# Performance work log

Hardware: AMD Instinct MI355X
Metric: run time of the kernel (lower is better)

The kernel has to match this reference:

```python
import jax, jax.numpy as jnp
import numpy as np

EMBED_DIM = 1024
NUM_HEADS = 8
SEQ_LEN = 2048
EPS = 1e-6


def setup_inputs() -> dict:
    key = jax.random.key(0)
    ks = jax.random.split(key, 8)
    E, NH, S = EMBED_DIM, NUM_HEADS, SEQ_LEN
    q = jax.random.normal(ks[0], (S, E), jnp.float32)
    k = jax.random.normal(ks[1], (S, E), jnp.float32)
    v = jax.random.normal(ks[2], (S, E), jnp.float32)
    # gate projections: weights init'd to zeros in the module; use small random
    # values so the gate math is exercised. Biases follow the module's init.
    Wi = 0.02 * jax.random.normal(ks[3], (NH, 3 * E), jnp.float32)
    bi = jnp.linspace(3.0, 6.0, NH, dtype=jnp.float32)
    Wf = 0.02 * jax.random.normal(ks[4], (NH, 3 * E), jnp.float32)
    bf = jnp.sqrt(0.1) * jax.random.normal(ks[5], (NH,), jnp.float32)
    # ResidualLayerNorm (xLSTM-style): effective scale = 1 + weight, no bias
    ln_weight = jnp.zeros((E,), jnp.float32)
    return {"q": q, "k": k, "v": v, "Wi": Wi, "bi": bi, "Wf": Wf, "bf": bf,
            "ln_weight": ln_weight}


def _mlstm_parallel(q, k, v, Wi, bi, Wf, bf, ln_weight):
    S, E = q.shape
    NH = Wi.shape[0]
    DH = E // NH
    gate_in = jnp.concatenate((q, k, v), axis=1)            # (S, 3E)
    ig = (gate_in @ Wi.T + bi).T[:, :, None]                # (NH, S, 1)
    fg = (gate_in @ Wf.T + bf).T[:, :, None]                # (NH, S, 1)

    qh = q.reshape(S, NH, DH).transpose(1, 0, 2)            # (NH, S, DH)
    kh = k.reshape(S, NH, DH).transpose(1, 0, 2)
    vh = v.reshape(S, NH, DH).transpose(1, 0, 2)

    # cumulative log forget gates
    log_f = jax.nn.log_sigmoid(fg)                          # (NH, S, 1)
    log_f_cum = jnp.concatenate(
        [jnp.zeros((NH, 1, 1), q.dtype), jnp.cumsum(log_f, axis=1)], axis=1
    )                                                       # (NH, S+1, 1)
    log_fg_mat = log_f_cum - log_f_cum.transpose(0, 2, 1)   # (NH, S+1, S+1)
    causal = jnp.tril(jnp.ones((S, S), bool))
    log_fg_mat = jnp.where(causal, log_fg_mat[:, 1:, 1:], -jnp.inf)  # (NH,S,S)

    log_D = log_fg_mat + ig.transpose(0, 2, 1)              # (NH, S, S)
    max_log_D = jnp.max(log_D, axis=-1, keepdims=True)      # (NH, S, 1)
    D = jnp.exp(log_D - max_log_D)                          # stabilized

    qk = jnp.einsum('hsd,htd->hst', qh, kh) / jnp.sqrt(jnp.asarray(DH, q.dtype))
    C = qk * D                                              # (NH, S, S)
    normalizer = jnp.maximum(jnp.abs(jnp.sum(C, axis=-1, keepdims=True)),
                             jnp.exp(-max_log_D))
    C_norm = C / (normalizer + EPS)
    h = jnp.einsum('hst,htd->hsd', C_norm, vh)              # (NH, S, DH)
    h = h.transpose(1, 0, 2).reshape(S, E)

    # residual layer norm: LN(h) * (1 + weight), no bias
    mu = jnp.mean(h, axis=-1, keepdims=True)
    var = jnp.mean(jnp.square(h - mu), axis=-1, keepdims=True)
    h_norm = (h - mu) * jax.lax.rsqrt(var + 1e-5)
    return h_norm * (1.0 + ln_weight)


def reference(q, k, v, Wi, bi, Wf, bf, ln_weight):
    return _mlstm_parallel(q, k, v, Wi, bi, Wf, bf, ln_weight)
```

## Files before the change

### kernel.cpp

```cpp
#include <hip/hip_runtime.h>
#include <math.h>

#define S_LEN 2048
#define EMB   1024
#define NHEAD 8
#define DH    128
#define E3    3072
#define BM    64
#define BN    32
#define NSPLIT 4
#define KSTRIDE  136
#define VTSTRIDE 40
#define PTSTRIDE 40

typedef __bf16 bf16x8 __attribute__((ext_vector_type(8)));
typedef __bf16 bf16x4 __attribute__((ext_vector_type(4)));
typedef float  f32x4  __attribute__((ext_vector_type(4)));

__global__ __launch_bounds__(256) void gates_cvt_transpose_kernel(
    const float* __restrict__ q, const float* __restrict__ k,
    const float* __restrict__ v,
    const float* __restrict__ Wi, const float* __restrict__ bi,
    const float* __restrict__ Wf, const float* __restrict__ bf,
    __bf16* __restrict__ Qh, __bf16* __restrict__ Ql,
    __bf16* __restrict__ Kh, __bf16* __restrict__ Kl,
    __bf16* __restrict__ Vt,
    float* __restrict__ ig, float* __restrict__ lf)
{
    const int tid = threadIdx.x;
    __shared__ union {
        float red[16][4];
        __bf16 tile[32][33];
    } sh;

    if (blockIdx.x < S_LEN) {
        const int t = blockIdx.x;
        const float4 qv = ((const float4*)q)[(size_t)t * 256 + tid];
        const float4 kv = ((const float4*)k)[(size_t)t * 256 + tid];
        const float4 vv = ((const float4*)v)[(size_t)t * 256 + tid];
        {
            size_t idx = (size_t)t * 256 + tid;
            bf16x4 hi, lo;
            hi[0]=(__bf16)qv.x; hi[1]=(__bf16)qv.y; hi[2]=(__bf16)qv.z; hi[3]=(__bf16)qv.w;
            lo[0]=(__bf16)(qv.x-(float)hi[0]); lo[1]=(__bf16)(qv.y-(float)hi[1]);
            lo[2]=(__bf16)(qv.z-(float)hi[2]); lo[3]=(__bf16)(qv.w-(float)hi[3]);
            ((bf16x4*)Qh)[idx] = hi; ((bf16x4*)Ql)[idx] = lo;
            hi[0]=(__bf16)kv.x; hi[1]=(__bf16)kv.y; hi[2]=(__bf16)kv.z; hi[3]=(__bf16)kv.w;
            lo[0]=(__bf16)(kv.x-(float)hi[0]); lo[1]=(__bf16)(kv.y-(float)hi[1]);
            lo[2]=(__bf16)(kv.z-(float)hi[2]); lo[3]=(__bf16)(kv.w-(float)hi[3]);
            ((bf16x4*)Kh)[idx] = hi; ((bf16x4*)Kl)[idx] = lo;
        }
        float acc[16];
        #pragma unroll
        for (int g = 0; g < 16; ++g) {
            const float4* w4 = (const float4*)((g < 8) ? (Wi + g * E3) : (Wf + (g - 8) * E3));
            float4 a = w4[tid], b = w4[256 + tid], c = w4[512 + tid];
            acc[g] = a.x*qv.x + a.y*qv.y + a.z*qv.z + a.w*qv.w
                   + b.x*kv.x + b.y*kv.y + b.z*kv.z + b.w*kv.w
                   + c.x*vv.x + c.y*vv.y + c.z*vv.z + c.w*vv.w;
        }
        const int w = tid >> 6, lane = tid & 63;
        #pragma unroll
        for (int g = 0; g < 16; ++g) {
            float x = acc[g];
            for (int o = 32; o > 0; o >>= 1) x += __shfl_down(x, o, 64);
            if (lane == 0) sh.red[g][w] = x;
        }
        __syncthreads();
        if (tid < 16) {
            float s = sh.red[tid][0] + sh.red[tid][1] + sh.red[tid][2] + sh.red[tid][3];
            if (tid < 8) {
                ig[tid * S_LEN + t] = s + bi[tid];
            } else {
                int h = tid - 8;
                float x = s + bf[h];
                lf[h * S_LEN + t] = fminf(x, 0.f) - log1pf(expf(-fabsf(x)));
            }
        }
    } else {
        const int tb = blockIdx.x - S_LEN;
        const int sb = (tb & 63) * 32, eb = (tb >> 6) * 32;
        #pragma unroll
        for (int i = 0; i < 4; ++i) {
            int lin = tid + i * 256;
            int sr = lin >> 5, ec = lin & 31;
            sh.tile[ec][sr] = (__bf16)v[(size_t)(sb + sr) * EMB + eb + ec];
        }
        __syncthreads();
        #pragma unroll
        for (int i = 0; i < 4; ++i) {
            int lin = tid + i * 256;
            int er = lin >> 5, sc = lin & 31;
            Vt[(size_t)(eb + er) * S_LEN + sb + sc] = sh.tile[er][sc];
        }
    }
}

__global__ __launch_bounds__(256) void cumsum_aux_kernel(
    const float* __restrict__ lf, const float* __restrict__ ig,
    float* __restrict__ F, float* __restrict__ ug,
    float* __restrict__ umax, float* __restrict__ upmax)
{
    const int h = blockIdx.x, tid = threadIdx.x;
    const int lane = tid & 63, w = tid >> 6;
    __shared__ float wsum[4];
    __shared__ float morig[256];
    float loc[8];
    const int base = tid * 8;
    float s = 0.f;
    for (int i = 0; i < 8; i++) { s += lf[h * S_LEN + base + i]; loc[i] = s; }
    float inc = s;
    #pragma unroll
    for (int o = 1; o < 64; o <<= 1) {
        float t = __shfl_up(inc, o, 64);
        if (lane >= o) inc += t;
    }
    if (lane == 63) wsum[w] = inc;
    __syncthreads();
    float wpre = 0.f;
    #pragma unroll
    for (int i = 0; i < 4; ++i) if (i < w) wpre += wsum[i];
    const float prev = wpre + inc - s;
    float* Fh = F + h * (S_LEN + 1);
    if (tid == 0) Fh[0] = 0.f;
    float Fv[8];
    for (int i = 0; i < 8; i++) { Fv[i] = prev + loc[i]; Fh[base + i + 1] = Fv[i]; }

    const float* igh = ig + h * S_LEN;
    float pm[8];
    float runm = -1e30f;
    #pragma unroll
    for (int i = 0; i < 8; i++) {
        float u = igh[base + i] - Fv[i];
        ug[h * S_LEN + base + i] = u;
        runm = fmaxf(runm, u);
        pm[i] = runm;
    }
    morig[tid] = runm;
    __syncthreads();
    const int g0 = tid & ~3;
    float pfx = -1e30f;
    for (int j = g0; j < tid; ++j) pfx = fmaxf(pfx, morig[j]);
    #pragma unroll
    for (int i = 0; i < 8; i++)
        upmax[h * S_LEN + base + i] = fmaxf(pfx, pm[i]);
    if ((tid & 3) == 0) {
        float mm = fmaxf(fmaxf(morig[tid], morig[tid + 1]),
                         fmaxf(morig[tid + 2], morig[tid + 3]));
        umax[h * 64 + (tid >> 2)] = mm;
    }
}

__global__ __launch_bounds__(256, 2) void mlstm_mfma(
    const __bf16* __restrict__ Qhg, const __bf16* __restrict__ Qlg,
    const __bf16* __restrict__ Khg, const __bf16* __restrict__ Klg,
    const __bf16* __restrict__ Vtg,
    const float* __restrict__ ug, const float* __restrict__ umaxg,
    const float* __restrict__ upmaxg, const float* __restrict__ F,
    __bf16* __restrict__ Opart, float* __restrict__ msplit,
    float* __restrict__ lsplit)
{
    const int flat = blockIdx.x;
    const int h = flat & 7;
    const int rest = flat >> 3;
    const int xx = rest & 15, z = rest >> 4;
    const int tid  = threadIdx.x;
    const int lane = tid & 63, w = tid >> 6;
    const int quad = lane >> 4, l15 = lane & 15;

    __shared__ __bf16 Kh[BN * KSTRIDE], Kl[BN * KSTRIDE];
    __shared__ __bf16 Vt[DH * VTSTRIDE];
    __shared__ __bf16 Pt[4][16 * PTSTRIDE];

    const float* Fh  = F  + h * (S_LEN + 1);
    const float* ugh = ug + h * S_LEN;
    const float scale = 0.088388347648318447f;
    const int kr  = tid >> 4, kc8 = tid & 15;
    const int vr0 = tid >> 2, vc0 = tid & 3;

    for (int pair = 0; pair < 2; ++pair) {
        const int qt = (pair == 0) ? xx : 31 - xx;
        const int qb = qt * BM;
        const int nj = 2 * qt + 2;
        const int j0 = (z * nj) / NSPLIT, j1 = ((z + 1) * nj) / NSPLIT;
        const int qbw = qb + w * 16;
        const int SBLK = (qb >> 5) + (w >> 1);

        float fq[4], upm[4];
        int sglob[4];
        #pragma unroll
        for (int r = 0; r < 4; ++r) {
            int s = qbw + quad * 4 + r;
            sglob[r] = s;
            fq[r]  = Fh[s + 1];
            upm[r] = upmaxg[h * S_LEN + s];
        }

        bf16x8 qh[4], ql[4];
        {
            const size_t qrow = (size_t)(qbw + l15) * EMB + h * DH + quad * 8;
            #pragma unroll
            for (int kk = 0; kk < 4; ++kk) {
                qh[kk] = *(const bf16x8*)(Qhg + qrow + kk * 32);
                ql[kk] = *(const bf16x8*)(Qlg + qrow + kk * 32);
            }
        }
        #pragma unroll
        for (int kk = 0; kk < 4; ++kk)
            asm volatile("" : "+v"(qh[kk]), "+v"(ql[kk]));

        float m_r[4] = {-1e30f, -1e30f, -1e30f, -1e30f};
        float l_r[4] = {0.f, 0.f, 0.f, 0.f};
        f32x4 Oacc[8] = {{0,0,0,0},{0,0,0,0},{0,0,0,0},{0,0,0,0},
                         {0,0,0,0},{0,0,0,0},{0,0,0,0},{0,0,0,0}};

        bf16x8 pk[2], pl[2], pv[2];
        float pu0 = 0.f, pu1 = 0.f, pum = 0.f;
        if (j0 < j1) {
            const int tb = j0 * BN;
            #pragma unroll
            for (int i = 0; i < 2; ++i) {
                int row = kr + 16 * i;
                size_t g = (size_t)(tb + row) * EMB + h * DH + kc8 * 8;
                pk[i] = *(const bf16x8*)(Khg + g);
                pl[i] = *(const bf16x8*)(Klg + g);
                pv[i] = *(const bf16x8*)(Vtg + (size_t)(h * DH + vr0 + 64 * i) * S_LEN + tb + vc0 * 8);
            }
            pu0 = ugh[tb + l15];
            pu1 = ugh[tb + 16 + l15];
            pum = umaxg[h * 64 + j0];
        }

        for (int j = j0; j < j1; ++j) {
            const int tb = j * BN;
            __syncthreads();
            #pragma unroll
            for (int i = 0; i < 2; ++i) {
                int row = kr + 16 * i;
                *(bf16x8*)&Kh[row * KSTRIDE + kc8 * 8] = pk[i];
                *(bf16x8*)&Kl[row * KSTRIDE + kc8 * 8] = pl[i];
                *(bf16x8*)&Vt[(vr0 + 64 * i) * VTSTRIDE + vc0 * 8] = pv[i];
            }
            __syncthreads();
            const float ut0 = pu0, ut1 = pu1, umj = pum;
            if (j + 1 < j1) {
                const int tb2 = tb + BN;
                #pragma unroll
                for (int i = 0; i < 2; ++i) {
                    int row = kr + 16 * i;
                    size_t g = (size_t)(tb2 + row) * EMB + h * DH + kc8 * 8;
                    pk[i] = *(const bf16x8*)(Khg + g);
                    pl[i] = *(const bf16x8*)(Klg + g);
                    pv[i] = *(const bf16x8*)(Vtg + (size_t)(h * DH + vr0 + 64 * i) * S_LEN + tb2 + vc0 * 8);
                }
                pu0 = ugh[tb2 + l15];
                pu1 = ugh[tb2 + 16 + l15];
                pum = umaxg[h * 64 + (j + 1)];
            }
            if (j <= SBLK) {
                f32x4 S0 = {0,0,0,0}, S1 = {0,0,0,0};
                #pragma unroll
                for (int kk = 0; kk < 4; ++kk) {
                    const int co = kk * 32 + quad * 8;
                    bf16x8 bh0 = *(const bf16x8*)&Kh[l15 * KSTRIDE + co];
                    bf16x8 bl0 = *(const bf16x8*)&Kl[l15 * KSTRIDE + co];
                    S0 = __builtin_amdgcn_mfma_f32_16x16x32_bf16(qh[kk], bh0, S0, 0, 0, 0);
                    S0 = __builtin_amdgcn_mfma_f32_16x16x32_bf16(qh[kk], bl0, S0, 0, 0, 0);
                    S0 = __builtin_amdgcn_mfma_f32_16x16x32_bf16(ql[kk], bh0, S0, 0, 0, 0);
                    bf16x8 bh1 = *(const bf16x8*)&Kh[(16 + l15) * KSTRIDE + co];
                    bf16x8 bl1 = *(const bf16x8*)&Kl[(16 + l15) * KSTRIDE + co];
                    S1 = __builtin_amdgcn_mfma_f32_16x16x32_bf16(qh[kk], bh1, S1, 0, 0, 0);
                    S1 = __builtin_amdgcn_mfma_f32_16x16x32_bf16(qh[kk], bl1, S1, 0, 0, 0);
                    S1 = __builtin_amdgcn_mfma_f32_16x16x32_bf16(ql[kk], bh1, S1, 0, 0, 0);
                }
                const int t0 = tb + l15, t1 = tb + 16 + l15;
                #pragma unroll
                for (int r = 0; r < 4; ++r) {
                    float mt = (j < SBLK) ? (fq[r] + umj) : (fq[r] + upm[r]);
                    float mn = fmaxf(m_r[r], mt);
                    float alpha = __expf(m_r[r] - mn);
                    m_r[r] = mn;
                    #pragma unroll
                    for (int nt = 0; nt < 8; ++nt) Oacc[nt][r] *= alpha;
                    float p0 = __expf(fq[r] + ut0 - mn) * S0[r] * scale;
                    float p1 = __expf(fq[r] + ut1 - mn) * S1[r] * scale;
                    if (j == SBLK) {
                        if (t0 > sglob[r]) p0 = 0.f;
                        if (t1 > sglob[r]) p1 = 0.f;
                    }
                    l_r[r] = l_r[r] * alpha + (p0 + p1);
                    const int prow = (quad * 4 + r) * PTSTRIDE;
                    Pt[w][prow + l15]      = (__bf16)p0;
                    Pt[w][prow + 16 + l15] = (__bf16)p1;
                }
                bf16x8 pa = *(const bf16x8*)&Pt[w][l15 * PTSTRIDE + quad * 8];
                #pragma unroll
                for (int nt = 0; nt < 8; ++nt) {
                    bf16x8 vb = *(const bf16x8*)&Vt[(nt * 16 + l15) * VTSTRIDE + quad * 8];
                    Oacc[nt] = __builtin_amdgcn_mfma_f32_16x16x32_bf16(pa, vb, Oacc[nt], 0, 0, 0);
                }
            }
        }
        __bf16* Oz = Opart + (size_t)z * S_LEN * EMB;
        #pragma unroll
        for (int nt = 0; nt < 8; ++nt) {
            #pragma unroll
            for (int r = 0; r < 4; ++r) {
                Oz[(size_t)sglob[r] * EMB + h * DH + nt * 16 + l15] = (__bf16)Oacc[nt][r];
            }
        }
        #pragma unroll
        for (int r = 0; r < 4; ++r) {
            float x = l_r[r];
            #pragma unroll
            for (int o = 1; o < 16; o <<= 1) x += __shfl_xor(x, o);
            l_r[r] = x;
        }
        if (l15 == 0) {
            #pragma unroll
            for (int r = 0; r < 4; ++r) {
                msplit[(z * NHEAD + h) * S_LEN + sglob[r]] = m_r[r];
                lsplit[(z * NHEAD + h) * S_LEN + sglob[r]] = l_r[r];
            }
        }
    }
}

__global__ __launch_bounds__(256) void combine_ln_kernel(
    const __bf16* __restrict__ Opart, const float* __restrict__ msplit,
    const float* __restrict__ lsplit, const float* __restrict__ lnw,
    float* __restrict__ out)
{
    const int tid = threadIdx.x;
    const int r  = tid >> 7;
    const int wr = (tid >> 6) & 1;
    const int c0 = (tid & 127) * 8;
    const int hh = c0 >> 7;
    const int s  = blockIdx.x * 2 + r;
    __shared__ float redsum[2][2], redvar[2][2];

    float m = -1e30f, es[NSPLIT], l = 0.f;
    #pragma unroll
    for (int zz = 0; zz < NSPLIT; ++zz)
        m = fmaxf(m, msplit[(zz * NHEAD + hh) * S_LEN + s]);
    #pragma unroll
    for (int zz = 0; zz < NSPLIT; ++zz) {
        es[zz] = __expf(msplit[(zz * NHEAD + hh) * S_LEN + s] - m);
        l += es[zz] * lsplit[(zz * NHEAD + hh) * S_LEN + s];
    }
    const float rn = 1.f / (fmaxf(fabsf(l), __expf(-m)) + 1e-6f);

    const size_t SE = (size_t)S_LEN * EMB;
    float x[8] = {0,0,0,0,0,0,0,0};
    #pragma unroll
    for (int zz = 0; zz < NSPLIT; ++zz) {
        bf16x8 o = *(const bf16x8*)(Opart + zz * SE + (size_t)s * EMB + c0);
        #pragma unroll
        for (int e = 0; e < 8; ++e) x[e] += es[zz] * (float)o[e];
    }
    float sum = 0.f;
    #pragma unroll
    for (int e = 0; e < 8; ++e) { x[e] *= rn; sum += x[e]; }
    for (int o = 32; o > 0; o >>= 1) sum += __shfl_down(sum, o, 64);
    if ((tid & 63) == 0) redsum[r][wr] = sum;
    __syncthreads();
    sum = redsum[r][0] + redsum[r][1];
    const float mu = sum * (1.f / EMB);
    float vs = 0.f;
    #pragma unroll
    for (int e = 0; e < 8; ++e) { float d = x[e] - mu; vs += d * d; }
    for (int o = 32; o > 0; o >>= 1) vs += __shfl_down(vs, o, 64);
    if ((tid & 63) == 0) redvar[r][wr] = vs;
    __syncthreads();
    vs = redvar[r][0] + redvar[r][1];
    const float rstd = rsqrtf(vs * (1.f / EMB) + 1e-5f);
    const float4 w0 = *(const float4*)(lnw + c0);
    const float4 w1 = *(const float4*)(lnw + c0 + 4);
    float4 o0, o1;
    o0.x = (x[0]-mu)*rstd*(1.f+w0.x); o0.y = (x[1]-mu)*rstd*(1.f+w0.y);
    o0.z = (x[2]-mu)*rstd*(1.f+w0.z); o0.w = (x[3]-mu)*rstd*(1.f+w0.w);
    o1.x = (x[4]-mu)*rstd*(1.f+w1.x); o1.y = (x[5]-mu)*rstd*(1.f+w1.y);
    o1.z = (x[6]-mu)*rstd*(1.f+w1.z); o1.w = (x[7]-mu)*rstd*(1.f+w1.w);
    *(float4*)(out + (size_t)s * EMB + c0)     = o0;
    *(float4*)(out + (size_t)s * EMB + c0 + 4) = o1;
}

extern "C" void kernel_launch(void* const* d_in, const int* in_sizes, int n_in,
                              void* d_out, int out_size, void* d_ws, size_t ws_size,
                              hipStream_t stream)
{
    const float* q   = (const float*)d_in[0];
    const float* k   = (const float*)d_in[1];
    const float* v   = (const float*)d_in[2];
    const float* Wi  = (const float*)d_in[3];
    const float* bi  = (const float*)d_in[4];
    const float* Wf  = (const float*)d_in[5];
    const float* bf  = (const float*)d_in[6];
    const float* lnw = (const float*)d_in[7];
    float* out = (float*)d_out;

    float* ws = (float*)d_ws;
    float* ig    = ws;
    float* lf    = ig + NHEAD * S_LEN;
    float* F     = lf + NHEAD * S_LEN;
    float* ugw   = F + NHEAD * (S_LEN + 1);
    float* umaxw = ugw + NHEAD * S_LEN;
    float* upmaxw= umaxw + NHEAD * 64;
    __bf16* Qh = (__bf16*)(upmaxw + NHEAD * S_LEN);
    const size_t SEb = (size_t)S_LEN * EMB;
    __bf16* Ql  = Qh + SEb;
    __bf16* Kh  = Ql + SEb;
    __bf16* Kl  = Kh + SEb;
    __bf16* Vtg = Kl + SEb;
    __bf16* Opart = Vtg + SEb;
    float* msplit = (float*)(Opart + (size_t)NSPLIT * SEb);
    float* lsplit = msplit + NSPLIT * NHEAD * S_LEN;

    gates_cvt_transpose_kernel<<<2 * S_LEN, 256, 0, stream>>>(
        q, k, v, Wi, bi, Wf, bf, Qh, Ql, Kh, Kl, Vtg, ig, lf);
    cumsum_aux_kernel<<<NHEAD, 256, 0, stream>>>(lf, ig, F, ugw, umaxw, upmaxw);
    mlstm_mfma<<<16 * NHEAD * NSPLIT, 256, 0, stream>>>(
        Qh, Ql, Kh, Kl, Vtg, ugw, umaxw, upmaxw, F, Opart, msplit, lsplit);
    combine_ln_kernel<<<S_LEN / 2, 256, 0, stream>>>(Opart, msplit, lsplit, lnw, out);
}
```

Baseline: 157.5 us.

## Fuse Q/K bf16 hi/lo split into attention kernel and double split count

The first kernel no longer writes bf16 hi/lo copies of Q and K. The MFMA attention kernel now reads fp32 Q and K directly and performs the hi/lo split in registers before staging K into shared memory. NSPLIT goes from 4 to 8, doubling the number of sequence-split blocks for more parallelism, at the cost of a larger partial-output buffer and more combine reads. The combine step skips loading partials whose scale factor is zero. The trade is less global write and read traffic for Q/K against doubled fp32 K loads and conversion work inside the attention loop.

```diff
diff --git a/kernel.cpp b/kernel.cpp
--- a/kernel.cpp
+++ b/kernel.cpp
@@ -8,7 +8,7 @@
 #define E3    3072
 #define BM    64
 #define BN    32
-#define NSPLIT 4
+#define NSPLIT 8
 #define KSTRIDE  136
 #define VTSTRIDE 40
 #define PTSTRIDE 40
@@ -22,8 +22,6 @@
     const float* __restrict__ v,
     const float* __restrict__ Wi, const float* __restrict__ bi,
     const float* __restrict__ Wf, const float* __restrict__ bf,
-    __bf16* __restrict__ Qh, __bf16* __restrict__ Ql,
-    __bf16* __restrict__ Kh, __bf16* __restrict__ Kl,
     __bf16* __restrict__ Vt,
     float* __restrict__ ig, float* __restrict__ lf)
 {
@@ -38,18 +36,6 @@
         const float4 qv = ((const float4*)q)[(size_t)t * 256 + tid];
         const float4 kv = ((const float4*)k)[(size_t)t * 256 + tid];
         const float4 vv = ((const float4*)v)[(size_t)t * 256 + tid];
-        {
-            size_t idx = (size_t)t * 256 + tid;
-            bf16x4 hi, lo;
-            hi[0]=(__bf16)qv.x; hi[1]=(__bf16)qv.y; hi[2]=(__bf16)qv.z; hi[3]=(__bf16)qv.w;
-            lo[0]=(__bf16)(qv.x-(float)hi[0]); lo[1]=(__bf16)(qv.y-(float)hi[1]);
-            lo[2]=(__bf16)(qv.z-(float)hi[2]); lo[3]=(__bf16)(qv.w-(float)hi[3]);
-            ((bf16x4*)Qh)[idx] = hi; ((bf16x4*)Ql)[idx] = lo;
-            hi[0]=(__bf16)kv.x; hi[1]=(__bf16)kv.y; hi[2]=(__bf16)kv.z; hi[3]=(__bf16)kv.w;
-            lo[0]=(__bf16)(kv.x-(float)hi[0]); lo[1]=(__bf16)(kv.y-(float)hi[1]);
-            lo[2]=(__bf16)(kv.z-(float)hi[2]); lo[3]=(__bf16)(kv.w-(float)hi[3]);
-            ((bf16x4*)Kh)[idx] = hi; ((bf16x4*)Kl)[idx] = lo;
-        }
         float acc[16];
         #pragma unroll
         for (int g = 0; g < 16; ++g) {
@@ -152,8 +138,7 @@
 }
 
 __global__ __launch_bounds__(256, 2) void mlstm_mfma(
-    const __bf16* __restrict__ Qhg, const __bf16* __restrict__ Qlg,
-    const __bf16* __restrict__ Khg, const __bf16* __restrict__ Klg,
+    const float* __restrict__ Qg, const float* __restrict__ Kg,
     const __bf16* __restrict__ Vtg,
     const float* __restrict__ ug, const float* __restrict__ umaxg,
     const float* __restrict__ upmaxg, const float* __restrict__ F,
@@ -198,11 +183,18 @@
 
         bf16x8 qh[4], ql[4];
         {
-            const size_t qrow = (size_t)(qbw + l15) * EMB + h * DH + quad * 8;
+            const float* qrowp = Qg + (size_t)(qbw + l15) * EMB + h * DH + quad * 8;
             #pragma unroll
             for (int kk = 0; kk < 4; ++kk) {
-                qh[kk] = *(const bf16x8*)(Qhg + qrow + kk * 32);
-                ql[kk] = *(const bf16x8*)(Qlg + qrow + kk * 32);
+                float4 a = *(const float4*)(qrowp + kk * 32);
+                float4 b = *(const float4*)(qrowp + kk * 32 + 4);
+                float f[8] = {a.x, a.y, a.z, a.w, b.x, b.y, b.z, b.w};
+                #pragma unroll
+                for (int e = 0; e < 8; ++e) {
+                    __bf16 hi = (__bf16)f[e];
+                    qh[kk][e] = hi;
+                    ql[kk][e] = (__bf16)(f[e] - (float)hi);
+                }
             }
         }
         #pragma unroll
@@ -214,16 +206,17 @@
         f32x4 Oacc[8] = {{0,0,0,0},{0,0,0,0},{0,0,0,0},{0,0,0,0},
                          {0,0,0,0},{0,0,0,0},{0,0,0,0},{0,0,0,0}};
 
-        bf16x8 pk[2], pl[2], pv[2];
+        float4 pkf[2][2];
+        bf16x8 pv[2];
         float pu0 = 0.f, pu1 = 0.f, pum = 0.f;
         if (j0 < j1) {
             const int tb = j0 * BN;
             #pragma unroll
             for (int i = 0; i < 2; ++i) {
                 int row = kr + 16 * i;
-                size_t g = (size_t)(tb + row) * EMB + h * DH + kc8 * 8;
-                pk[i] = *(const bf16x8*)(Khg + g);
-                pl[i] = *(const bf16x8*)(Klg + g);
+                const float* gp = Kg + (size_t)(tb + row) * EMB + h * DH + kc8 * 8;
+                pkf[i][0] = *(const float4*)(gp);
+                pkf[i][1] = *(const float4*)(gp + 4);
                 pv[i] = *(const bf16x8*)(Vtg + (size_t)(h * DH + vr0 + 64 * i) * S_LEN + tb + vc0 * 8);
             }
             pu0 = ugh[tb + l15];
@@ -237,8 +230,17 @@
             #pragma unroll
             for (int i = 0; i < 2; ++i) {
                 int row = kr + 16 * i;
-                *(bf16x8*)&Kh[row * KSTRIDE + kc8 * 8] = pk[i];
-                *(bf16x8*)&Kl[row * KSTRIDE + kc8 * 8] = pl[i];
+                float f[8] = {pkf[i][0].x, pkf[i][0].y, pkf[i][0].z, pkf[i][0].w,
+                              pkf[i][1].x, pkf[i][1].y, pkf[i][1].z, pkf[i][1].w};
+                bf16x8 hi, lo;
+                #pragma unroll
+                for (int e = 0; e < 8; ++e) {
+                    __bf16 hb = (__bf16)f[e];
+                    hi[e] = hb;
+                    lo[e] = (__bf16)(f[e] - (float)hb);
+                }
+                *(bf16x8*)&Kh[row * KSTRIDE + kc8 * 8] = hi;
+                *(bf16x8*)&Kl[row * KSTRIDE + kc8 * 8] = lo;
                 *(bf16x8*)&Vt[(vr0 + 64 * i) * VTSTRIDE + vc0 * 8] = pv[i];
             }
             __syncthreads();
@@ -248,9 +250,9 @@
                 #pragma unroll
                 for (int i = 0; i < 2; ++i) {
                     int row = kr + 16 * i;
-                    size_t g = (size_t)(tb2 + row) * EMB + h * DH + kc8 * 8;
-                    pk[i] = *(const bf16x8*)(Khg + g);
-                    pl[i] = *(const bf16x8*)(Klg + g);
+                    const float* gp = Kg + (size_t)(tb2 + row) * EMB + h * DH + kc8 * 8;
+                    pkf[i][0] = *(const float4*)(gp);
+                    pkf[i][1] = *(const float4*)(gp + 4);
                     pv[i] = *(const bf16x8*)(Vtg + (size_t)(h * DH + vr0 + 64 * i) * S_LEN + tb2 + vc0 * 8);
                 }
                 pu0 = ugh[tb2 + l15];
@@ -354,9 +356,11 @@
     float x[8] = {0,0,0,0,0,0,0,0};
     #pragma unroll
     for (int zz = 0; zz < NSPLIT; ++zz) {
-        bf16x8 o = *(const bf16x8*)(Opart + zz * SE + (size_t)s * EMB + c0);
-        #pragma unroll
-        for (int e = 0; e < 8; ++e) x[e] += es[zz] * (float)o[e];
+        if (es[zz] != 0.f) {
+            bf16x8 o = *(const bf16x8*)(Opart + zz * SE + (size_t)s * EMB + c0);
+            #pragma unroll
+            for (int e = 0; e < 8; ++e) x[e] += es[zz] * (float)o[e];
+        }
     }
     float sum = 0.f;
     #pragma unroll
@@ -406,20 +410,16 @@
     float* ugw   = F + NHEAD * (S_LEN + 1);
     float* umaxw = ugw + NHEAD * S_LEN;
     float* upmaxw= umaxw + NHEAD * 64;
-    __bf16* Qh = (__bf16*)(upmaxw + NHEAD * S_LEN);
+    __bf16* Vtg = (__bf16*)(upmaxw + NHEAD * S_LEN);
     const size_t SEb = (size_t)S_LEN * EMB;
-    __bf16* Ql  = Qh + SEb;
-    __bf16* Kh  = Ql + SEb;
-    __bf16* Kl  = Kh + SEb;
-    __bf16* Vtg = Kl + SEb;
     __bf16* Opart = Vtg + SEb;
     float* msplit = (float*)(Opart + (size_t)NSPLIT * SEb);
     float* lsplit = msplit + NSPLIT * NHEAD * S_LEN;
 
     gates_cvt_transpose_kernel<<<2 * S_LEN, 256, 0, stream>>>(
-        q, k, v, Wi, bi, Wf, bf, Qh, Ql, Kh, Kl, Vtg, ig, lf);
+        q, k, v, Wi, bi, Wf, bf, Vtg, ig, lf);
     cumsum_aux_kernel<<<NHEAD, 256, 0, stream>>>(lf, ig, F, ugw, umaxw, upmaxw);
     mlstm_mfma<<<16 * NHEAD * NSPLIT, 256, 0, stream>>>(
-        Qh, Ql, Kh, Kl, Vtg, ugw, umaxw, upmaxw, F, Opart, msplit, lsplit);
+        q, k, Vtg, ugw, umaxw, upmaxw, F, Opart, msplit, lsplit);
     combine_ln_kernel<<<S_LEN / 2, 256, 0, stream>>>(Opart, msplit, lsplit, lnw, out);
 }
```

After: 162.8 us. 1.03x slower.

## Stream K/V tiles via direct global-to-LDS loads with double buffering and XOR swizzle

Applied to the files above, without the earlier changes.

Replaces register-staged K/V loads followed by LDS stores with global_load_lds direct copies into double-buffered LDS, cutting one barrier per iteration and freeing the registers that held the prefetch. Padded LDS strides give way to XOR-swizzled layouts to avoid bank conflicts. The combine kernel also skips loading split partials whose weight is zero. LDS use roughly doubles, and correctness depends on the async load being complete at the trailing barrier.

```diff
diff --git a/kernel.cpp b/kernel.cpp
--- a/kernel.cpp
+++ b/kernel.cpp
@@ -9,13 +9,17 @@
 #define BM    64
 #define BN    32
 #define NSPLIT 4
-#define KSTRIDE  136
-#define VTSTRIDE 40
 #define PTSTRIDE 40
 
 typedef __bf16 bf16x8 __attribute__((ext_vector_type(8)));
 typedef __bf16 bf16x4 __attribute__((ext_vector_type(4)));
 typedef float  f32x4  __attribute__((ext_vector_type(4)));
+
+__device__ __forceinline__ void gload16(const __bf16* g, __bf16* l) {
+    __builtin_amdgcn_global_load_lds(
+        (const __attribute__((address_space(1))) void*)g,
+        (__attribute__((address_space(3))) void*)l, 16, 0, 0);
+}
 
 __global__ __launch_bounds__(256) void gates_cvt_transpose_kernel(
     const float* __restrict__ q, const float* __restrict__ k,
@@ -168,15 +172,34 @@
     const int lane = tid & 63, w = tid >> 6;
     const int quad = lane >> 4, l15 = lane & 15;
 
-    __shared__ __bf16 Kh[BN * KSTRIDE], Kl[BN * KSTRIDE];
-    __shared__ __bf16 Vt[DH * VTSTRIDE];
+    __shared__ __bf16 KhL[2][4096];
+    __shared__ __bf16 KlL[2][4096];
+    __shared__ __bf16 VtL[2][4096];
     __shared__ __bf16 Pt[4][16 * PTSTRIDE];
 
     const float* Fh  = F  + h * (S_LEN + 1);
     const float* ugh = ug + h * S_LEN;
     const float scale = 0.088388347648318447f;
-    const int kr  = tid >> 4, kc8 = tid & 15;
-    const int vr0 = tid >> 2, vc0 = tid & 3;
+
+    const int krow0 = tid >> 4;
+    const int krow1 = 16 + krow0;
+    const int kchk  = (tid & 15) ^ (krow0 & 15);
+    const int vrow0 = tid >> 2;
+    const int vrow1 = 64 + vrow0;
+    const int vchk  = (tid & 3) ^ ((vrow0 ^ (vrow0 >> 2)) & 3);
+    const int ldsw  = w * 512;
+
+#define STAGE(B, TB) do {                                                     \
+    const __bf16* kb_ = Khg + (size_t)(TB) * EMB + h * DH;                    \
+    const __bf16* lb_ = Klg + (size_t)(TB) * EMB + h * DH;                    \
+    const __bf16* vg_ = Vtg + (size_t)(h * DH) * S_LEN + (TB);                \
+    gload16(kb_ + (size_t)krow0 * EMB + kchk * 8, &KhL[B][ldsw]);             \
+    gload16(kb_ + (size_t)krow1 * EMB + kchk * 8, &KhL[B][2048 + ldsw]);      \
+    gload16(lb_ + (size_t)krow0 * EMB + kchk * 8, &KlL[B][ldsw]);             \
+    gload16(lb_ + (size_t)krow1 * EMB + kchk * 8, &KlL[B][2048 + ldsw]);      \
+    gload16(vg_ + (size_t)vrow0 * S_LEN + vchk * 8, &VtL[B][ldsw]);           \
+    gload16(vg_ + (size_t)vrow1 * S_LEN + vchk * 8, &VtL[B][2048 + ldsw]);    \
+} while (0)
 
     for (int pair = 0; pair < 2; ++pair) {
         const int qt = (pair == 0) ? xx : 31 - xx;
@@ -214,61 +237,37 @@
         f32x4 Oacc[8] = {{0,0,0,0},{0,0,0,0},{0,0,0,0},{0,0,0,0},
                          {0,0,0,0},{0,0,0,0},{0,0,0,0},{0,0,0,0}};
 
-        bf16x8 pk[2], pl[2], pv[2];
         float pu0 = 0.f, pu1 = 0.f, pum = 0.f;
+        int buf = 0;
         if (j0 < j1) {
-            const int tb = j0 * BN;
-            #pragma unroll
-            for (int i = 0; i < 2; ++i) {
-                int row = kr + 16 * i;
-                size_t g = (size_t)(tb + row) * EMB + h * DH + kc8 * 8;
-                pk[i] = *(const bf16x8*)(Khg + g);
-                pl[i] = *(const bf16x8*)(Klg + g);
-                pv[i] = *(const bf16x8*)(Vtg + (size_t)(h * DH + vr0 + 64 * i) * S_LEN + tb + vc0 * 8);
-            }
-            pu0 = ugh[tb + l15];
-            pu1 = ugh[tb + 16 + l15];
+            STAGE(0, j0 * BN);
+            pu0 = ugh[j0 * BN + l15];
+            pu1 = ugh[j0 * BN + 16 + l15];
             pum = umaxg[h * 64 + j0];
+            __syncthreads();
         }
 
         for (int j = j0; j < j1; ++j) {
             const int tb = j * BN;
-            __syncthreads();
-            #pragma unroll
-            for (int i = 0; i < 2; ++i) {
-                int row = kr + 16 * i;
-                *(bf16x8*)&Kh[row * KSTRIDE + kc8 * 8] = pk[i];
-                *(bf16x8*)&Kl[row * KSTRIDE + kc8 * 8] = pl[i];
-                *(bf16x8*)&Vt[(vr0 + 64 * i) * VTSTRIDE + vc0 * 8] = pv[i];
-            }
-            __syncthreads();
             const float ut0 = pu0, ut1 = pu1, umj = pum;
             if (j + 1 < j1) {
-                const int tb2 = tb + BN;
-                #pragma unroll
-                for (int i = 0; i < 2; ++i) {
-                    int row = kr + 16 * i;
-                    size_t g = (size_t)(tb2 + row) * EMB + h * DH + kc8 * 8;
-                    pk[i] = *(const bf16x8*)(Khg + g);
-                    pl[i] = *(const bf16x8*)(Klg + g);
-                    pv[i] = *(const bf16x8*)(Vtg + (size_t)(h * DH + vr0 + 64 * i) * S_LEN + tb2 + vc0 * 8);
-                }
-                pu0 = ugh[tb2 + l15];
-                pu1 = ugh[tb2 + 16 + l15];
+                STAGE(buf ^ 1, tb + BN);
+                pu0 = ugh[tb + BN + l15];
+                pu1 = ugh[tb + BN + 16 + l15];
                 pum = umaxg[h * 64 + (j + 1)];
             }
             if (j <= SBLK) {
                 f32x4 S0 = {0,0,0,0}, S1 = {0,0,0,0};
                 #pragma unroll
                 for (int kk = 0; kk < 4; ++kk) {
-                    const int co = kk * 32 + quad * 8;
-                    bf16x8 bh0 = *(const bf16x8*)&Kh[l15 * KSTRIDE + co];
-                    bf16x8 bl0 = *(const bf16x8*)&Kl[l15 * KSTRIDE + co];
+                    const int kpos = (((kk << 2) | quad) ^ l15) * 8;
+                    bf16x8 bh0 = *(const bf16x8*)&KhL[buf][l15 * 128 + kpos];
+                    bf16x8 bl0 = *(const bf16x8*)&KlL[buf][l15 * 128 + kpos];
                     S0 = __builtin_amdgcn_mfma_f32_16x16x32_bf16(qh[kk], bh0, S0, 0, 0, 0);
                     S0 = __builtin_amdgcn_mfma_f32_16x16x32_bf16(qh[kk], bl0, S0, 0, 0, 0);
                     S0 = __builtin_amdgcn_mfma_f32_16x16x32_bf16(ql[kk], bh0, S0, 0, 0, 0);
-                    bf16x8 bh1 = *(const bf16x8*)&Kh[(16 + l15) * KSTRIDE + co];
-                    bf16x8 bl1 = *(const bf16x8*)&Kl[(16 + l15) * KSTRIDE + co];
+                    bf16x8 bh1 = *(const bf16x8*)&KhL[buf][(16 + l15) * 128 + kpos];
+                    bf16x8 bl1 = *(const bf16x8*)&KlL[buf][(16 + l15) * 128 + kpos];
                     S1 = __builtin_amdgcn_mfma_f32_16x16x32_bf16(qh[kk], bh1, S1, 0, 0, 0);
                     S1 = __builtin_amdgcn_mfma_f32_16x16x32_bf16(qh[kk], bl1, S1, 0, 0, 0);
                     S1 = __builtin_amdgcn_mfma_f32_16x16x32_bf16(ql[kk], bh1, S1, 0, 0, 0);
@@ -296,10 +295,14 @@
                 bf16x8 pa = *(const bf16x8*)&Pt[w][l15 * PTSTRIDE + quad * 8];
                 #pragma unroll
                 for (int nt = 0; nt < 8; ++nt) {
-                    bf16x8 vb = *(const bf16x8*)&Vt[(nt * 16 + l15) * VTSTRIDE + quad * 8];
-                    Oacc[nt] = __builtin_amdgcn_mfma_f32_16x16x32_bf16(pa, vb, Oacc[nt], 0, 0, 0);
+                    const int vrow = nt * 16 + l15;
+                    const int vpos = (quad ^ ((vrow ^ (vrow >> 2)) & 3)) * 8;
+                    bf16x8 vv = *(const bf16x8*)&VtL[buf][vrow * 32 + vpos];
+                    Oacc[nt] = __builtin_amdgcn_mfma_f32_16x16x32_bf16(pa, vv, Oacc[nt], 0, 0, 0);
                 }
             }
+            __syncthreads();
+            buf ^= 1;
         }
         __bf16* Oz = Opart + (size_t)z * S_LEN * EMB;
         #pragma unroll
@@ -324,6 +327,7 @@
             }
         }
     }
+#undef STAGE
 }
 
 __global__ __launch_bounds__(256) void combine_ln_kernel(
@@ -354,9 +358,11 @@
     float x[8] = {0,0,0,0,0,0,0,0};
     #pragma unroll
     for (int zz = 0; zz < NSPLIT; ++zz) {
-        bf16x8 o = *(const bf16x8*)(Opart + zz * SE + (size_t)s * EMB + c0);
-        #pragma unroll
-        for (int e = 0; e < 8; ++e) x[e] += es[zz] * (float)o[e];
+        if (es[zz] != 0.f) {
+            bf16x8 o = *(const bf16x8*)(Opart + zz * SE + (size_t)s * EMB + c0);
+            #pragma unroll
+            for (int e = 0; e < 8; ++e) x[e] += es[zz] * (float)o[e];
+        }
     }
     float sum = 0.f;
     #pragma unroll
```

New measurement: 155.9 us. No clear change (-1.0%).
